# Optimization experiments

Hardware: AMD Instinct MI355X
Metric: run time of the kernel (lower is better)

Reference implementation:

```python
import jax, jax.numpy as jnp
import numpy as np

B, T, C = 16, 1024, 1024
H = 4          # wshare
K = 31         # kernel_size


def setup_inputs() -> dict:
    key = jax.random.key(0)
    ks = jax.random.split(key, 8)
    s = 1.0 / np.sqrt(C)
    return {
        "query": jax.random.normal(ks[0], (B, T, C), jnp.float32),
        "key_t": jax.random.normal(ks[1], (B, T, C), jnp.float32),   # unused, API compat
        "value": jax.random.normal(ks[2], (B, T, C), jnp.float32),   # unused, API compat
        "mask": jnp.ones((B, 1, T), jnp.int32),
        "W1": jax.random.uniform(ks[3], (2 * C, C), jnp.float32, -s, s),
        "b1": jnp.zeros((2 * C,), jnp.float32),
        "W2": jax.random.uniform(ks[4], (C, C), jnp.float32, -s, s),
        "b2": jnp.zeros((C,), jnp.float32),
        "conv_w": jax.random.uniform(ks[5], (H, K), jnp.float32, 0.0, 1.0),
        "bias": jnp.zeros((C,), jnp.float32),
    }


def reference(query, key_t, value, mask, W1, b1, W2, b2, conv_w, bias):
    # linear1 + GLU: (B,T,C) -> (B,T,2C) -> (B,T,C)
    x = query @ W1.T + b1
    a, g = jnp.split(x, 2, axis=-1)
    x = a * jax.nn.sigmoid(g)
    # (B,T,C) -> (B,C,T) -> (B*C/H, H, T); channel c uses shared kernel c % H
    x = jnp.transpose(x, (0, 2, 1)).reshape(B * C // H, H, T)
    # softmax-normalized shared kernels (H,K); dropout_rate=0 (eval)
    w = jax.nn.softmax(conv_w, axis=-1)
    y = jax.lax.conv_general_dilated(
        x, w[:, None, :], window_strides=(1,), padding=[(K // 2, K // 2)],
        feature_group_count=H, dimension_numbers=("NCH", "OIH", "NCH"))
    x = y.reshape(B, C, T) + bias[None, :, None]
    x = jnp.transpose(x, (0, 2, 1))               # (B,T,C)
    # padding mask: (B,1,T) -> transpose(-1,-2) -> (B,T,1), zero masked frames
    m = jnp.transpose(mask, (0, 2, 1))
    x = jnp.where(m == 0, 0.0, x)
    return x @ W2.T + b2
```

## Files before the change

kernel.cpp:

```cpp
#include <hip/hip_runtime.h>

typedef __attribute__((ext_vector_type(8))) __bf16 bf16x8;
typedef __attribute__((ext_vector_type(4))) __bf16 bf16x4;
typedef __attribute__((ext_vector_type(4))) float  f32x4;
typedef __attribute__((ext_vector_type(4))) float  float4v;

#define DEV static __device__ __forceinline__

DEV void gload_lds16(const void* g, void* l) {
  __builtin_amdgcn_global_load_lds(
      (const __attribute__((address_space(1))) void*)g,
      (__attribute__((address_space(3))) void*)l, 16, 0, 0);
}

__global__ void cvt_bf16_kernel(const float* __restrict__ in,
                                __bf16* __restrict__ out, int n4) {
  int stride = gridDim.x * blockDim.x;
  for (int i = blockIdx.x * blockDim.x + threadIdx.x; i < n4; i += stride) {
    float4v v = ((const float4v*)in)[i];
    bf16x4 o;
#pragma unroll
    for (int j = 0; j < 4; ++j) o[j] = (__bf16)v[j];
    ((bf16x4*)out)[i] = o;
  }
}

__global__ void prep_all_kernel(const float* __restrict__ W1, const float* __restrict__ W2,
                                const float* __restrict__ cw, const float* __restrict__ b1,
                                __bf16* __restrict__ w1p, __bf16* __restrict__ w2b,
                                float* __restrict__ swm, float* __restrict__ b1p) {
  const int blk = blockIdx.x;
  const int tid = threadIdx.x;
  if (blk < 1024) {
    const int r   = blk * 2 + (tid >> 7);
    const int col = (tid & 127) * 8;
    const int g  = r >> 8, p = r & 255;
    const int wn = p >> 6, jj = (p >> 4) & 3, c16 = p & 15;
    const int ch = g * 128 + wn * 32 + (jj & 1) * 16 + c16;
    const int src = ch + (jj >= 2 ? 1024 : 0);
    const float* ptr = W1 + (long)src * 1024 + col;
    float4v v0 = *(const float4v*)ptr;
    float4v v1 = *(const float4v*)(ptr + 4);
    bf16x8 o;
#pragma unroll
    for (int j = 0; j < 4; ++j) { o[j] = (__bf16)v0[j]; o[4 + j] = (__bf16)v1[j]; }
    *(bf16x8*)(w1p + (long)r * 1024 + col) = o;
  } else if (blk < 1280) {
    int i = (blk - 1024) * 256 + tid;
#pragma unroll 4
    for (; i < 262144; i += 65536) {
      float4v v = ((const float4v*)W2)[i];
      bf16x4 o;
#pragma unroll
      for (int j = 0; j < 4; ++j) o[j] = (__bf16)v[j];
      ((bf16x4*)w2b)[i] = o;
    }
  } else {
    if (tid < 4) {
      const int h = tid;
      float m = cw[h * 31];
#pragma unroll
      for (int k = 1; k < 31; ++k) m = fmaxf(m, cw[h * 31 + k]);
      float e[31];
      float s = 0.f;
#pragma unroll
      for (int k = 0; k < 31; ++k) {
        e[k] = __expf(cw[h * 31 + k] - m);
        s += e[k];
      }
      float inv = 1.f / s;
#pragma unroll
      for (int k = 0; k < 31; ++k) swm[h * 31 + k] = e[k] * inv;
    }
    for (int i = tid; i < 2048; i += 256) {
      const int g = i >> 8, p = i & 255;
      const int wn = p >> 6, jj = (p >> 4) & 3, c16 = p & 15;
      const int ch = g * 128 + wn * 32 + (jj & 1) * 16 + c16;
      b1p[i] = b1[ch + (jj >= 2 ? 1024 : 0)];
    }
  }
}

template <int MODE>
DEV void gemm_body(const __bf16* __restrict__ A, const __bf16* __restrict__ Bw,
                   const float* __restrict__ bias, void* __restrict__ Cout,
                   int M, int N, int K, int ntn) {
  __shared__ __align__(16) __bf16 Al[4 * 8192];
  __shared__ __align__(16) __bf16 Bl[4 * 8192];

  const int tid  = threadIdx.x;
  const int lane = tid & 63;
  const int w    = tid >> 6;
  const int wm = w >> 2, wn = w & 3;

  const int nwg = gridDim.x;
  const int cpx = nwg >> 3;
  const int bid = blockIdx.x;
  const int wgid = (bid & 7) * cpx + (bid >> 3);
  const int m0 = (wgid / ntn) * 256;
  const int n0 = (wgid % ntn) * 256;

  const int NT = K >> 6;

  const int scolE = ((((tid & 7) * 16) ^ (((tid >> 3) & 7) << 4)) >> 1);
  const __bf16* __restrict__ Abase = A + (long)m0 * K;
  const __bf16* __restrict__ Bbase = Bw + (long)n0 * K;

  const int l15 = lane & 15;
  const int xk  = (l15 & 7) << 4;
  const int a0  = l15 * 128 + (((lane >> 4) * 16) ^ xk);
  const int a1  = l15 * 128 + ((((lane >> 4) * 16) + 64) ^ xk);
  const int bq  = (wn & 1) * 8192;
  const int b0  = bq + a0;
  const int b1r = bq + a1;

  f32x4 acc[8][4];
#pragma unroll
  for (int i = 0; i < 8; ++i)
#pragma unroll
    for (int j = 0; j < 4; ++j) {
      acc[i][j][0] = 0.f; acc[i][j][1] = 0.f;
      acc[i][j][2] = 0.f; acc[i][j][3] = 0.f;
    }
  bf16x8 af[8], bf[8];

#define ADST(p, mh) (Al + ((p) * 2 + (mh)) * 8192)
#define BDST(p, nh) (Bl + ((p) * 2 + (nh)) * 8192)
#define AWG(p) ((const char*)Al + ((p) * 2 + wm) * 16384)
#define BWG(p) ((const char*)Bl + ((p) * 2 + (wn >> 1)) * 16384)

#define STAGEG(base, groff, ktc, dst)                                             \
  {                                                                               \
    const __bf16* _s = (base) + (long)((groff) + (tid >> 3)) * K + (ktc) + scolE; \
    gload_lds16(_s, (dst) + tid * 8);                                             \
    gload_lds16(_s + (long)64 * K, (dst) + 4096 + tid * 8);                       \
  }

#define PH_MID()                                     \
  __builtin_amdgcn_s_barrier();                      \
  asm volatile("s_waitcnt lgkmcnt(0)" ::: "memory"); \
  __builtin_amdgcn_s_setprio(1);

#define PH_END(VM)                                                    \
  __builtin_amdgcn_s_setprio(0);                                      \
  if ((VM) == 4) asm volatile("s_waitcnt vmcnt(4)" ::: "memory");     \
  if ((VM) == 0) asm volatile("s_waitcnt vmcnt(0)" ::: "memory");     \
  __builtin_amdgcn_s_barrier();

#define RDA(IB, G)                                                    \
  _Pragma("unroll") for (int i2 = 0; i2 < 4; ++i2) {                  \
    af[i2 * 2 + 0] = *(const bf16x8*)((G) + ((IB) + i2) * 2048 + a0); \
    af[i2 * 2 + 1] = *(const bf16x8*)((G) + ((IB) + i2) * 2048 + a1); \
  }
#define RDB(JB, G)                                                                \
  _Pragma("unroll") for (int j2 = 0; j2 < 2; ++j2) {                              \
    bf[(JB) * 2 + j2 * 2 + 0] = *(const bf16x8*)((G) + ((JB) + j2) * 2048 + b0);  \
    bf[(JB) * 2 + j2 * 2 + 1] = *(const bf16x8*)((G) + ((JB) + j2) * 2048 + b1r); \
  }

#define MMQ(IB, JB)                                                           \
  _Pragma("unroll") for (int i2 = 0; i2 < 4; ++i2)                            \
  _Pragma("unroll") for (int j2 = 0; j2 < 2; ++j2)                            \
  _Pragma("unroll") for (int kk = 0; kk < 2; ++kk)                            \
      acc[(IB) + i2][(JB) + j2] = __builtin_amdgcn_mfma_f32_16x16x32_bf16(    \
          af[i2 * 2 + kk], bf[(JB) * 2 + j2 * 2 + kk], acc[(IB) + i2][(JB) + j2], 0, 0, 0);

  STAGEG(Abase, 0,   0, ADST(0, 0));
  STAGEG(Abase, 128, 0, ADST(0, 1));
  STAGEG(Bbase, 0,   0, BDST(0, 0));
  STAGEG(Bbase, 128, 0, BDST(0, 1));
  asm volatile("s_waitcnt vmcnt(0)" ::: "memory");
  __builtin_amdgcn_s_barrier();

#define TILE(tt, CUR)                                           \
  {                                                             \
    const int ktn = (((tt) + 1 < NT) ? (tt) + 1 : NT - 1) * 64; \
    RDA(0, AWG(CUR)); RDB(0, BWG(CUR));                         \
    STAGEG(Abase, 0,   ktn, ADST(CUR ^ 1, 0));                  \
    STAGEG(Abase, 128, ktn, ADST(CUR ^ 1, 1));                  \
    PH_MID(); MMQ(0, 0); PH_END(9);                             \
    RDB(2, BWG(CUR));                                           \
    STAGEG(Bbase, 0,   ktn, BDST(CUR ^ 1, 0));                  \
    STAGEG(Bbase, 128, ktn, BDST(CUR ^ 1, 1));                  \
    PH_MID(); MMQ(0, 2); PH_END(9);                             \
    RDA(4, AWG(CUR));                                           \
    PH_MID(); MMQ(4, 0); PH_END(4);                             \
    PH_MID(); MMQ(4, 2); PH_END(0);                             \
  }

#pragma unroll 1
  for (int t2 = 0; t2 < NT; t2 += 2) {
    TILE(t2, 0);
    TILE(t2 + 1, 1);
  }

  asm volatile("s_waitcnt vmcnt(0)" ::: "memory");

  const int crow = (lane >> 4) * 4;
  const int ccol = lane & 15;
  if (MODE == 0) {
#pragma unroll
    for (int i = 0; i < 8; ++i) {
      const int mrow = m0 + wm * 128 + i * 16 + crow;
#pragma unroll
      for (int j = 0; j < 4; ++j) {
        const int ncol = n0 + wn * 64 + j * 16 + ccol;
        const float bv = bias[ncol];
#pragma unroll
        for (int r = 0; r < 4; ++r)
          ((float*)Cout)[(long)(mrow + r) * N + ncol] = acc[i][j][r] + bv;
      }
    }
  } else {
    __builtin_amdgcn_s_barrier();
    __bf16* wa = (__bf16*)Al + w * 640;
    const int chbase = (n0 >> 1) + wn * 32;
    const int rr = lane >> 2, c8 = (lane & 3) * 8;
#pragma unroll
    for (int i = 0; i < 8; ++i) {
#pragma unroll
      for (int j = 0; j < 2; ++j) {
        const int na = n0 + wn * 64 + j * 16 + ccol;
        const float bva = bias[na];
        const float bvg = bias[na + 32];
#pragma unroll
        for (int r = 0; r < 4; ++r) {
          float a = acc[i][j][r] + bva;
          float gv = acc[i][j + 2][r] + bvg;
          float res = a * __builtin_amdgcn_rcpf(1.f + __expf(-gv));
          wa[(crow + r) * 40 + j * 16 + ccol] = (__bf16)res;
        }
      }
      bf16x8 v = *(const bf16x8*)(wa + rr * 40 + c8);
      const int gr = m0 + wm * 128 + i * 16 + rr;
      *(bf16x8*)((__bf16*)Cout + (long)gr * (N >> 1) + chbase + c8) = v;
    }
  }
#undef TILE
#undef STAGEG
#undef PH_MID
#undef PH_END
#undef RDA
#undef RDB
#undef MMQ
#undef ADST
#undef BDST
#undef AWG
#undef BWG
}

__global__ __launch_bounds__(512, 2)
void gemm1_glu_kernel(const __bf16* __restrict__ A, const __bf16* __restrict__ Bw,
                      const float* __restrict__ bias, void* __restrict__ Cout,
                      int M, int N, int K, int ntn) {
  gemm_body<1>(A, Bw, bias, Cout, M, N, K, ntn);
}

__global__ __launch_bounds__(512, 2)
void gemm2_out_kernel(const __bf16* __restrict__ A, const __bf16* __restrict__ Bw,
                      const float* __restrict__ bias, void* __restrict__ Cout,
                      int M, int N, int K, int ntn) {
  gemm_body<0>(A, Bw, bias, Cout, M, N, K, ntn);
}

__global__ __launch_bounds__(256, 2)
void conv_kernel(const __bf16* __restrict__ Yin, const float* __restrict__ Wsm,
                 const float* __restrict__ bias, const int* __restrict__ mask,
                 __bf16* __restrict__ Y) {
  const int b  = blockIdx.z;
  const int t0 = blockIdx.y * 64;
  const int c0 = blockIdx.x * 128;
  __shared__ float sgT[128][128];
  __shared__ float swl[124];
  const int tid = threadIdx.x;
  if (tid < 124) swl[tid] = Wsm[tid];

  for (int i = tid; i < 2048; i += 256) {
    const int ttl = i & 127;
    const int cg  = i >> 7;
    if (ttl < 94) {
      const int t = t0 - 15 + ttl;
      float v[8];
      if (t >= 0 && t < 1024) {
        bf16x8 a8 = *(const bf16x8*)(Yin + ((long)(b * 1024 + t)) * 1024 + c0 + cg * 8);
#pragma unroll
        for (int j = 0; j < 8; ++j) v[j] = (float)a8[j];
      } else {
#pragma unroll
        for (int j = 0; j < 8; ++j) v[j] = 0.f;
      }
      const int q = ttl >> 2, e = ttl & 3;
#pragma unroll
      for (int j = 0; j < 8; ++j) {
        const int c = cg * 8 + j;
        sgT[c][((q ^ ((c & 7) << 2)) << 2) + e] = v[j];
      }
    }
  }
  __syncthreads();

  const int cc = tid & 127;
  const int th = tid >> 7;
  const int c  = c0 + cc;
  const float* wrow = swl + (c & 3) * 31;
  const float bv = bias[c];
  float acc[32];
#pragma unroll
  for (int u = 0; u < 32; ++u) acc[u] = bv;
  const int key = (cc & 7) << 2;
#pragma unroll
  for (int qi = 0; qi < 16; ++qi) {
    const int q = th * 8 + qi;
    const f32x4 w4 = *(const f32x4*)&sgT[cc][(q ^ key) << 2];
#pragma unroll
    for (int j = 0; j < 4; ++j) {
      const int rl = qi * 4 + j;
#pragma unroll
      for (int u = 0; u < 32; ++u) {
        const int k = rl - u;
        if (k >= 0 && k < 31) acc[u] += w4[j] * wrow[k];
      }
    }
  }
  const long yb = (long)b * 1024 * 1024;
#pragma unroll
  for (int u = 0; u < 32; ++u) {
    const int gt = t0 + th * 32 + u;
    float v = acc[u];
    if (mask[b * 1024 + gt] == 0) v = 0.f;
    Y[yb + (long)gt * 1024 + c] = (__bf16)v;
  }
}

extern "C" void kernel_launch(void* const* d_in, const int* in_sizes, int n_in,
                              void* d_out, int out_size, void* d_ws, size_t ws_size,
                              hipStream_t stream) {
  const float* q    = (const float*)d_in[0];
  const int*   mask = (const int*)d_in[3];
  const float* W1   = (const float*)d_in[4];
  const float* b1   = (const float*)d_in[5];
  const float* W2   = (const float*)d_in[6];
  const float* b2   = (const float*)d_in[7];
  const float* cw   = (const float*)d_in[8];
  const float* bias = (const float*)d_in[9];

  char* ws = (char*)d_ws;
  __bf16* q_bf  = (__bf16*)(ws);
  __bf16* w1p   = (__bf16*)(ws + (32u << 20));
  __bf16* w2_bf = (__bf16*)(ws + (36u << 20));
  float*  swm   = (float*)(ws + (38u << 20));
  float*  b1p   = (float*)(ws + (38u << 20) + 4096);
  __bf16* y     = (__bf16*)d_out;
  __bf16* yc    = q_bf;

  cvt_bf16_kernel<<<2048, 256, 0, stream>>>(q, q_bf, 16 * 1024 * 1024 / 4);
  prep_all_kernel<<<1281, 256, 0, stream>>>(W1, W2, cw, b1, w1p, w2_bf, swm, b1p);

  gemm1_glu_kernel<<<512, 512, 0, stream>>>(q_bf, w1p, b1p, (void*)y,
                                            16384, 2048, 1024, 8);
  conv_kernel<<<dim3(8, 16, 16), 256, 0, stream>>>(y, swm, bias, mask, yc);
  gemm2_out_kernel<<<256, 512, 0, stream>>>(yc, w2_bf, b2, d_out,
                                            16384, 1024, 1024, 4);
}
```

Before: 163.1 us.

## Triple-buffer A tiles in GEMM pipeline and fuse bf16 conversion into prep kernel

The GEMM main loop changes from double-buffered A/B with a two-tile unrolled body to a rotating three-slot A buffer plus a two-slot B buffer. A is prefetched two K-steps ahead and B one step ahead, so most phases no longer wait on vmcnt. LDS use grows to 160 KB per block, and launch bounds drop to one block per CU, which loses occupancy in exchange for deeper prefetch. The separate query-to-bf16 conversion kernel is also folded into the prep kernel, saving one launch.

```diff
diff --git a/kernel.cpp b/kernel.cpp
--- a/kernel.cpp
+++ b/kernel.cpp
@@ -13,26 +13,26 @@
       (__attribute__((address_space(3))) void*)l, 16, 0, 0);
 }
 
-__global__ void cvt_bf16_kernel(const float* __restrict__ in,
-                                __bf16* __restrict__ out, int n4) {
-  int stride = gridDim.x * blockDim.x;
-  for (int i = blockIdx.x * blockDim.x + threadIdx.x; i < n4; i += stride) {
-    float4v v = ((const float4v*)in)[i];
-    bf16x4 o;
-#pragma unroll
-    for (int j = 0; j < 4; ++j) o[j] = (__bf16)v[j];
-    ((bf16x4*)out)[i] = o;
-  }
-}
-
-__global__ void prep_all_kernel(const float* __restrict__ W1, const float* __restrict__ W2,
-                                const float* __restrict__ cw, const float* __restrict__ b1,
-                                __bf16* __restrict__ w1p, __bf16* __restrict__ w2b,
+__global__ void prep_all_kernel(const float* __restrict__ q, const float* __restrict__ W1,
+                                const float* __restrict__ W2, const float* __restrict__ cw,
+                                const float* __restrict__ b1,
+                                __bf16* __restrict__ qb, __bf16* __restrict__ w1p,
+                                __bf16* __restrict__ w2b,
                                 float* __restrict__ swm, float* __restrict__ b1p) {
   const int blk = blockIdx.x;
   const int tid = threadIdx.x;
-  if (blk < 1024) {
-    const int r   = blk * 2 + (tid >> 7);
+  if (blk < 2048) {
+    int i = blk * 256 + tid;
+#pragma unroll 8
+    for (int it = 0; it < 8; ++it, i += 524288) {
+      float4v v = ((const float4v*)q)[i];
+      bf16x4 o;
+#pragma unroll
+      for (int j = 0; j < 4; ++j) o[j] = (__bf16)v[j];
+      ((bf16x4*)qb)[i] = o;
+    }
+  } else if (blk < 3072) {
+    const int r   = (blk - 2048) * 2 + (tid >> 7);
     const int col = (tid & 127) * 8;
     const int g  = r >> 8, p = r & 255;
     const int wn = p >> 6, jj = (p >> 4) & 3, c16 = p & 15;
@@ -45,10 +45,10 @@
 #pragma unroll
     for (int j = 0; j < 4; ++j) { o[j] = (__bf16)v0[j]; o[4 + j] = (__bf16)v1[j]; }
     *(bf16x8*)(w1p + (long)r * 1024 + col) = o;
-  } else if (blk < 1280) {
-    int i = (blk - 1024) * 256 + tid;
+  } else if (blk < 3328) {
+    int i = (blk - 3072) * 256 + tid;
 #pragma unroll 4
-    for (; i < 262144; i += 65536) {
+    for (int it = 0; it < 4; ++it, i += 65536) {
       float4v v = ((const float4v*)W2)[i];
       bf16x4 o;
 #pragma unroll
@@ -85,8 +85,8 @@
 DEV void gemm_body(const __bf16* __restrict__ A, const __bf16* __restrict__ Bw,
                    const float* __restrict__ bias, void* __restrict__ Cout,
                    int M, int N, int K, int ntn) {
-  __shared__ __align__(16) __bf16 Al[4 * 8192];
-  __shared__ __align__(16) __bf16 Bl[4 * 8192];
+  __shared__ __align__(16) __bf16 Al[3 * 16384];
+  __shared__ __align__(16) __bf16 Bl[2 * 16384];
 
   const int tid  = threadIdx.x;
   const int lane = tid & 63;
@@ -124,11 +124,6 @@
     }
   bf16x8 af[8], bf[8];
 
-#define ADST(p, mh) (Al + ((p) * 2 + (mh)) * 8192)
-#define BDST(p, nh) (Bl + ((p) * 2 + (nh)) * 8192)
-#define AWG(p) ((const char*)Al + ((p) * 2 + wm) * 16384)
-#define BWG(p) ((const char*)Bl + ((p) * 2 + (wn >> 1)) * 16384)
-
 #define STAGEG(base, groff, ktc, dst)                                             \
   {                                                                               \
     const __bf16* _s = (base) + (long)((groff) + (tid >> 3)) * K + (ktc) + scolE; \
@@ -141,10 +136,13 @@
   asm volatile("s_waitcnt lgkmcnt(0)" ::: "memory"); \
   __builtin_amdgcn_s_setprio(1);
 
-#define PH_END(VM)                                                    \
-  __builtin_amdgcn_s_setprio(0);                                      \
-  if ((VM) == 4) asm volatile("s_waitcnt vmcnt(4)" ::: "memory");     \
-  if ((VM) == 0) asm volatile("s_waitcnt vmcnt(0)" ::: "memory");     \
+#define PH_ENDN()                                    \
+  __builtin_amdgcn_s_setprio(0);                     \
+  __builtin_amdgcn_s_barrier();
+
+#define PH_END4()                                    \
+  __builtin_amdgcn_s_setprio(0);                     \
+  asm volatile("s_waitcnt vmcnt(4)" ::: "memory");   \
   __builtin_amdgcn_s_barrier();
 
 #define RDA(IB, G)                                                    \
@@ -165,33 +163,43 @@
       acc[(IB) + i2][(JB) + j2] = __builtin_amdgcn_mfma_f32_16x16x32_bf16(    \
           af[i2 * 2 + kk], bf[(JB) * 2 + j2 * 2 + kk], acc[(IB) + i2][(JB) + j2], 0, 0, 0);
 
-  STAGEG(Abase, 0,   0, ADST(0, 0));
-  STAGEG(Abase, 128, 0, ADST(0, 1));
-  STAGEG(Bbase, 0,   0, BDST(0, 0));
-  STAGEG(Bbase, 128, 0, BDST(0, 1));
-  asm volatile("s_waitcnt vmcnt(0)" ::: "memory");
+  __bf16* aRd = Al;
+  __bf16* aNx = Al + 16384;
+  __bf16* aSt = Al + 32768;
+  __bf16* bRd = Bl;
+  __bf16* bSt = Bl + 16384;
+
+  STAGEG(Abase, 0,   0, aRd);
+  STAGEG(Abase, 128, 0, aRd + 8192);
+  STAGEG(Bbase, 0,   0, bRd);
+  STAGEG(Bbase, 128, 0, bRd + 8192);
+  {
+    const int k1 = (1 < NT ? 1 : NT - 1) * 64;
+    STAGEG(Abase, 0,   k1, aNx);
+    STAGEG(Abase, 128, k1, aNx + 8192);
+  }
+  asm volatile("s_waitcnt vmcnt(4)" ::: "memory");
   __builtin_amdgcn_s_barrier();
 
-#define TILE(tt, CUR)                                           \
-  {                                                             \
-    const int ktn = (((tt) + 1 < NT) ? (tt) + 1 : NT - 1) * 64; \
-    RDA(0, AWG(CUR)); RDB(0, BWG(CUR));                         \
-    STAGEG(Abase, 0,   ktn, ADST(CUR ^ 1, 0));                  \
-    STAGEG(Abase, 128, ktn, ADST(CUR ^ 1, 1));                  \
-    PH_MID(); MMQ(0, 0); PH_END(9);                             \
-    RDB(2, BWG(CUR));                                           \
-    STAGEG(Bbase, 0,   ktn, BDST(CUR ^ 1, 0));                  \
-    STAGEG(Bbase, 128, ktn, BDST(CUR ^ 1, 1));                  \
-    PH_MID(); MMQ(0, 2); PH_END(9);                             \
-    RDA(4, AWG(CUR));                                           \
-    PH_MID(); MMQ(4, 0); PH_END(4);                             \
-    PH_MID(); MMQ(4, 2); PH_END(0);                             \
-  }
-
 #pragma unroll 1
-  for (int t2 = 0; t2 < NT; t2 += 2) {
-    TILE(t2, 0);
-    TILE(t2 + 1, 1);
+  for (int t = 0; t < NT; ++t) {
+    const int kB = ((t + 1 < NT) ? t + 1 : NT - 1) * 64;
+    const int kA = ((t + 2 < NT) ? t + 2 : NT - 1) * 64;
+    const char* aG = (const char*)aRd + wm * 16384;
+    const char* bG = (const char*)bRd + (wn >> 1) * 16384;
+    RDA(0, aG); RDB(0, bG);
+    STAGEG(Bbase, 0,   kB, bSt);
+    STAGEG(Bbase, 128, kB, bSt + 8192);
+    PH_MID(); MMQ(0, 0); PH_ENDN();
+    RDB(2, bG);
+    STAGEG(Abase, 0,   kA, aSt);
+    STAGEG(Abase, 128, kA, aSt + 8192);
+    PH_MID(); MMQ(0, 2); PH_ENDN();
+    RDA(4, aG);
+    PH_MID(); MMQ(4, 0); PH_ENDN();
+    PH_MID(); MMQ(4, 2); PH_END4();
+    __bf16* ta = aRd; aRd = aNx; aNx = aSt; aSt = ta;
+    __bf16* tb = bRd; bRd = bSt; bSt = tb;
   }
 
   asm volatile("s_waitcnt vmcnt(0)" ::: "memory");
@@ -236,27 +244,23 @@
       *(bf16x8*)((__bf16*)Cout + (long)gr * (N >> 1) + chbase + c8) = v;
     }
   }
-#undef TILE
 #undef STAGEG
 #undef PH_MID
-#undef PH_END
+#undef PH_ENDN
+#undef PH_END4
 #undef RDA
 #undef RDB
 #undef MMQ
-#undef ADST
-#undef BDST
-#undef AWG
-#undef BWG
-}
-
-__global__ __launch_bounds__(512, 2)
+}
+
+__global__ __launch_bounds__(512, 1)
 void gemm1_glu_kernel(const __bf16* __restrict__ A, const __bf16* __restrict__ Bw,
                       const float* __restrict__ bias, void* __restrict__ Cout,
                       int M, int N, int K, int ntn) {
   gemm_body<1>(A, Bw, bias, Cout, M, N, K, ntn);
 }
 
-__global__ __launch_bounds__(512, 2)
+__global__ __launch_bounds__(512, 1)
 void gemm2_out_kernel(const __bf16* __restrict__ A, const __bf16* __restrict__ Bw,
                       const float* __restrict__ bias, void* __restrict__ Cout,
                       int M, int N, int K, int ntn) {
@@ -353,8 +357,8 @@
   __bf16* y     = (__bf16*)d_out;
   __bf16* yc    = q_bf;
 
-  cvt_bf16_kernel<<<2048, 256, 0, stream>>>(q, q_bf, 16 * 1024 * 1024 / 4);
-  prep_all_kernel<<<1281, 256, 0, stream>>>(W1, W2, cw, b1, w1p, w2_bf, swm, b1p);
+  prep_all_kernel<<<3329, 256, 0, stream>>>(q, W1, W2, cw, b1,
+                                            q_bf, w1p, w2_bf, swm, b1p);
 
   gemm1_glu_kernel<<<512, 512, 0, stream>>>(q_bf, w1p, b1p, (void*)y,
                                             16384, 2048, 1024, 8);
```

Result: faster. 157.6 us (-3.4%).
